# Optimization experiments

Measured on AMD Instinct MI355X. Metric: run time of the kernel, lower is better.

Reference implementation:

```python
import jax, jax.numpy as jnp
import numpy as np

N = 50000
D = 128           # feature_dim
H = 8             # num_heads
DH = D // H       # head_dim = 16
K = 32            # k_neighbors
FFN = int(D * 1.5)  # 192
TAU_NEG = 0.6
BETA = 1.5
LN_EPS = 1e-5


def layer_norm(x, g, b):
    mu = jnp.mean(x, axis=-1, keepdims=True)
    var = jnp.mean((x - mu) ** 2, axis=-1, keepdims=True)
    return (x - mu) * jax.lax.rsqrt(var + LN_EPS) * g + b


def setup_inputs() -> dict:
    key = jax.random.key(0)
    ks = jax.random.split(key, 12)
    s = 1.0 / np.sqrt(D)
    inp = {
        "features": jax.random.normal(ks[0], (N, D), dtype=jnp.float32),
        "knn_indices": jax.random.randint(ks[1], (N, K), 0, N, dtype=jnp.int64 if jax.config.jax_enable_x64 else jnp.int32),
        "spatial_distances": jax.random.uniform(ks[2], (N, K), dtype=jnp.float32) * 8.0,
        "Wq": jax.random.normal(ks[3], (D, D), dtype=jnp.float32) * s,
        "Wk": jax.random.normal(ks[4], (D, D), dtype=jnp.float32) * s,
        "Wv": jax.random.normal(ks[5], (D, D), dtype=jnp.float32) * s,
        "Wo": jax.random.normal(ks[6], (D, D), dtype=jnp.float32) * s,
        "bo": jnp.zeros((D,), dtype=jnp.float32),
        "ln1_g": jnp.ones((D,), dtype=jnp.float32),
        "ln1_b": jnp.zeros((D,), dtype=jnp.float32),
        "W1": jax.random.normal(ks[7], (D, FFN), dtype=jnp.float32) * s,
        "b1": jnp.zeros((FFN,), dtype=jnp.float32),
        "W2": jax.random.normal(ks[8], (FFN, D), dtype=jnp.float32) * (1.0 / np.sqrt(FFN)),
        "b2": jnp.zeros((D,), dtype=jnp.float32),
        "ln2_g": jnp.ones((D,), dtype=jnp.float32),
        "ln2_b": jnp.zeros((D,), dtype=jnp.float32),
    }
    return inp


def reference(features, knn_indices, spatial_distances, Wq, Wk, Wv, Wo, bo,
              ln1_g, ln1_b, W1, b1, W2, b2, ln2_g, ln2_b):
    n = features.shape[0]
    Q = (features @ Wq).reshape(n, H, DH)           # (N,H,dh)
    Kp = (features @ Wk).reshape(n, H, DH)
    Vp = (features @ Wv).reshape(n, H, DH)

    K_local = Kp[knn_indices]                        # (N,K,H,dh) irregular gather
    V_local = Vp[knn_indices]                        # (N,K,H,dh)

    raw_scores = jnp.einsum("nhd,nkhd->nhk", Q, K_local) / np.sqrt(DH)  # (N,H,K)

    # per-head spatial decay: 1 / 2^(h+1)
    head_scalings = (0.5 ** jnp.arange(1, H + 1, dtype=features.dtype))  # (H,)
    scaled_dist = spatial_distances[:, None, :] * head_scalings[None, :, None]  # (N,H,K)

    attn_pos = jax.nn.softmax(raw_scores - scaled_dist, axis=-1)
    attn_neg = jax.nn.softmax((-raw_scores - scaled_dist) / TAU_NEG, axis=-1)
    attn = attn_pos - BETA * attn_neg                # (N,H,K); dropout is identity in eval

    attended = jnp.einsum("nhk,nkhd->nhd", attn, V_local).reshape(n, D)

    x = attended @ Wo + bo + features
    x = layer_norm(x, ln1_g, ln1_b)

    h = jax.nn.gelu(x @ W1 + b1, approximate=False)
    ffn_out = h @ W2 + b2
    out = layer_norm(ffn_out + x, ln2_g, ln2_b)
    return out
```

## Files before the change

### kernel.cpp

```cpp
#include <hip/hip_runtime.h>
#include <hip/hip_fp16.h>
#include <cmath>

typedef __attribute__((ext_vector_type(8))) _Float16 f16x8;
typedef __attribute__((ext_vector_type(4))) float f32x4;

__device__ __forceinline__ unsigned int pkh(float a, float b) {
    __half2 h = __floats2half2_rn(a, b);
    return *(unsigned int*)&h;
}
__device__ __forceinline__ float gelu_exact(float v) {
    return 0.5f * v * (1.0f + erff(v * 0.70710678118654752440f));
}
__device__ __forceinline__ __half2 shfl8h(__half2 x, int m) {
    int xi = *(int*)&x;
    int yi = __shfl_xor(xi, m, 8);
    return *(__half2*)&yi;
}

__global__ __launch_bounds__(256, 1) void k_prep(
    const float* __restrict__ Wq, const float* __restrict__ Wk, const float* __restrict__ Wv,
    const float* __restrict__ Wo, const float* __restrict__ W1, const float* __restrict__ W2,
    unsigned short* __restrict__ wsz)
{
    int f = blockIdx.x * 256 + threadIdx.x;
    const float* W; unsigned short* dst; int M, KS, fl;
    if (f < 2048)       { W = Wq; dst = wsz;         M = 128; KS = 4; fl = f; }
    else if (f < 4096)  { W = Wk; dst = wsz + 16384; M = 128; KS = 4; fl = f - 2048; }
    else if (f < 6144)  { W = Wv; dst = wsz + 32768; M = 128; KS = 4; fl = f - 4096; }
    else if (f < 8192)  { W = Wo; dst = wsz + 49152; M = 128; KS = 4; fl = f - 6144; }
    else if (f < 11264) { W = W1; dst = wsz + 65536; M = 192; KS = 4; fl = f - 8192; }
    else if (f < 14336) { W = W2; dst = wsz + 90112; M = 128; KS = 6; fl = f - 11264; }
    else return;
    const int l  = fl & 63;
    const int ks = (fl >> 6) % KS;
    const int ct = (fl >> 6) / KS;
    const int k0 = ks * 32 + (l >> 4) * 8;
    const int col = ct * 16 + (l & 15);
    unsigned short tmp[8];
    #pragma unroll
    for (int j = 0; j < 8; ++j) {
        __half hh = __float2half(W[(size_t)(k0 + j) * M + col]);
        tmp[j] = *(unsigned short*)&hh;
    }
    ((uint4*)dst)[fl] = *(uint4*)tmp;
}

__global__ __launch_bounds__(256, 4) void k_qkv(
    const float* __restrict__ feat, const unsigned short* __restrict__ wsz,
    unsigned short* __restrict__ Qb, unsigned short* __restrict__ Kb,
    unsigned short* __restrict__ Vb, int n)
{
    const int w = threadIdx.x >> 6, lane = threadIdx.x & 63;
    const int lrow = lane & 15, kgrp = lane >> 4;
    const int node = blockIdx.x * 64 + w * 16 + lrow;
    const bool valid = node < n;

    f16x8 bfr[4];
    #pragma unroll
    for (int ks = 0; ks < 4; ++ks) {
        float4 lo = make_float4(0.f, 0.f, 0.f, 0.f), hi = lo;
        if (valid) {
            const float* p = feat + (size_t)node * 128 + ks * 32 + kgrp * 8;
            lo = *(const float4*)p;
            hi = *(const float4*)(p + 4);
        }
        f16x8 b;
        b[0] = (_Float16)lo.x; b[1] = (_Float16)lo.y; b[2] = (_Float16)lo.z; b[3] = (_Float16)lo.w;
        b[4] = (_Float16)hi.x; b[5] = (_Float16)hi.y; b[6] = (_Float16)hi.z; b[7] = (_Float16)hi.w;
        bfr[ks] = b;
    }

    for (int mat = 0; mat < 3; ++mat) {
        const unsigned short* wb = wsz + mat * 16384;
        f32x4 acc[8];
        #pragma unroll
        for (int ct = 0; ct < 8; ++ct) acc[ct] = (f32x4){0.f, 0.f, 0.f, 0.f};
        #pragma unroll
        for (int ct = 0; ct < 8; ++ct)
            #pragma unroll
            for (int ks = 0; ks < 4; ++ks) {
                f16x8 afr = *(const f16x8*)(wb + ((size_t)(ct * 4 + ks) * 64 + lane) * 8);
                acc[ct] = __builtin_amdgcn_mfma_f32_16x16x32_f16(afr, bfr[ks], acc[ct], 0, 0, 0);
            }
        unsigned short* O = (mat == 0) ? Qb : (mat == 1 ? Kb : Vb);
        if (valid) {
            #pragma unroll
            for (int ct = 0; ct < 8; ++ct) {
                int col = ct * 16 + kgrp * 4;
                *((uint2*)(O + (size_t)node * 128 + col)) =
                    make_uint2(pkh(acc[ct][0], acc[ct][1]), pkh(acc[ct][2], acc[ct][3]));
            }
        }
    }
}

__global__ __launch_bounds__(256, 4) void k_attn(
    const unsigned short* __restrict__ Qb, const unsigned short* __restrict__ Kb,
    const unsigned short* __restrict__ Vb,
    const int* __restrict__ knn, const float* __restrict__ dist,
    unsigned short* __restrict__ attb, int n)
{
    const int lane = threadIdx.x & 63;
    const int node = blockIdx.x * 4 + (threadIdx.x >> 6);
    if (node >= n) return;
    const int h = lane >> 3, r = lane & 7;
    const float hs = exp2f(-(float)(h + 1));

    int idx[4]; float sd[4];
    #pragma unroll
    for (int jj = 0; jj < 4; ++jj) {
        int j = r + jj * 8;
        idx[jj] = knn[(size_t)node * 32 + j];
        sd[jj]  = dist[(size_t)node * 32 + j] * hs;
    }

    const unsigned short* qp = Qb + (size_t)node * 128 + h * 16;
    __half2 q2[8];
    *((uint4*)&q2[0]) = *(const uint4*)qp;
    *((uint4*)&q2[4]) = *(const uint4*)(qp + 8);

    uint4 k0[4], k1[4], v0[4], v1[4];
    #pragma unroll
    for (int jj = 0; jj < 4; ++jj) {
        const unsigned short* kp = Kb + (size_t)idx[jj] * 128 + h * 16;
        k0[jj] = *(const uint4*)kp;
        k1[jj] = *(const uint4*)(kp + 8);
    }
    #pragma unroll
    for (int jj = 0; jj < 4; ++jj) {
        const unsigned short* vp = Vb + (size_t)idx[jj] * 128 + h * 16;
        v0[jj] = *(const uint4*)vp;
        v1[jj] = *(const uint4*)(vp + 8);
    }

    float ap[4], an[4];
    #pragma unroll
    for (int jj = 0; jj < 4; ++jj) {
        const __half2* ka = (const __half2*)&k0[jj];
        const __half2* kb = (const __half2*)&k1[jj];
        __half2 s0 = __hmul2(q2[0], ka[0]);
        s0 = __hfma2(q2[1], ka[1], s0);
        s0 = __hfma2(q2[2], ka[2], s0);
        s0 = __hfma2(q2[3], ka[3], s0);
        __half2 s1 = __hmul2(q2[4], kb[0]);
        s1 = __hfma2(q2[5], kb[1], s1);
        s1 = __hfma2(q2[6], kb[2], s1);
        s1 = __hfma2(q2[7], kb[3], s1);
        float s = __low2float(s0) + __high2float(s0) + __low2float(s1) + __high2float(s1);
        float raw = s * 0.25f;
        ap[jj] = raw - sd[jj];
        an[jj] = (-raw - sd[jj]) * (1.0f / 0.6f);
    }

    float mp = fmaxf(fmaxf(ap[0], ap[1]), fmaxf(ap[2], ap[3]));
    float mn = fmaxf(fmaxf(an[0], an[1]), fmaxf(an[2], an[3]));
    #pragma unroll
    for (int msk = 1; msk < 8; msk <<= 1) {
        mp = fmaxf(mp, __shfl_xor(mp, msk, 8));
        mn = fmaxf(mn, __shfl_xor(mn, msk, 8));
    }
    float ep[4], en[4], sp = 0.f, sn = 0.f;
    #pragma unroll
    for (int jj = 0; jj < 4; ++jj) {
        ep[jj] = expf(ap[jj] - mp); sp += ep[jj];
        en[jj] = expf(an[jj] - mn); sn += en[jj];
    }
    #pragma unroll
    for (int msk = 1; msk < 8; msk <<= 1) {
        sp += __shfl_xor(sp, msk, 8);
        sn += __shfl_xor(sn, msk, 8);
    }
    const float isp = 1.0f / sp;
    const float isn = 1.5f / sn;

    __half2 acc2[8];
    #pragma unroll
    for (int i = 0; i < 8; ++i) acc2[i] = __float2half2_rn(0.f);
    #pragma unroll
    for (int jj = 0; jj < 4; ++jj) {
        float wgt = ep[jj] * isp - en[jj] * isn;
        __half2 w2 = __float2half2_rn(wgt);
        const __half2* va = (const __half2*)&v0[jj];
        const __half2* vb = (const __half2*)&v1[jj];
        acc2[0] = __hfma2(w2, va[0], acc2[0]);
        acc2[1] = __hfma2(w2, va[1], acc2[1]);
        acc2[2] = __hfma2(w2, va[2], acc2[2]);
        acc2[3] = __hfma2(w2, va[3], acc2[3]);
        acc2[4] = __hfma2(w2, vb[0], acc2[4]);
        acc2[5] = __hfma2(w2, vb[1], acc2[5]);
        acc2[6] = __hfma2(w2, vb[2], acc2[6]);
        acc2[7] = __hfma2(w2, vb[3], acc2[7]);
    }
    #pragma unroll
    for (int i = 0; i < 8; ++i) {
        acc2[i] = __hadd2(acc2[i], shfl8h(acc2[i], 1));
        acc2[i] = __hadd2(acc2[i], shfl8h(acc2[i], 2));
        acc2[i] = __hadd2(acc2[i], shfl8h(acc2[i], 4));
    }
    if (r == 0) {
        unsigned short* op = attb + (size_t)node * 128 + h * 16;
        *((uint4*)op)       = *(uint4*)&acc2[0];
        *((uint4*)(op + 8)) = *(uint4*)&acc2[4];
    }
}

__global__ __launch_bounds__(512, 1) void k_tail1(
    const unsigned short* __restrict__ attb, const float* __restrict__ feat,
    const unsigned short* __restrict__ wsz,
    const float* __restrict__ bo, const float* __restrict__ g1, const float* __restrict__ b1ln,
    unsigned short* __restrict__ Xb, int n)
{
    __shared__ __align__(16) unsigned short wo_s[16384];
    const int tid = threadIdx.x;
    for (int i = tid; i < 2048; i += 512)
        ((uint4*)wo_s)[i] = ((const uint4*)(wsz + 49152))[i];

    const int w = tid >> 6, lane = tid & 63;
    const int lrow = lane & 15, kgrp = lane >> 4;
    const int node = blockIdx.x * 128 + w * 16 + lrow;
    const bool valid = node < n;

    f16x8 bfr[4];
    #pragma unroll
    for (int ks = 0; ks < 4; ++ks) {
        uint4 u = make_uint4(0u, 0u, 0u, 0u);
        if (valid) u = *(const uint4*)(attb + (size_t)node * 128 + ks * 32 + kgrp * 8);
        bfr[ks] = *(f16x8*)&u;
    }
    __syncthreads();

    f32x4 X[8];
    #pragma unroll
    for (int ct = 0; ct < 8; ++ct) {
        X[ct] = (f32x4){0.f, 0.f, 0.f, 0.f};
        #pragma unroll
        for (int ks = 0; ks < 4; ++ks) {
            f16x8 afr = *(const f16x8*)&wo_s[((ct * 4 + ks) * 64 + lane) * 8];
            X[ct] = __builtin_amdgcn_mfma_f32_16x16x32_f16(afr, bfr[ks], X[ct], 0, 0, 0);
        }
    }
    #pragma unroll
    for (int ct = 0; ct < 8; ++ct) {
        int col = ct * 16 + kgrp * 4;
        float4 bv = *((const float4*)(bo + col));
        float4 fr = make_float4(0.f, 0.f, 0.f, 0.f);
        if (valid) fr = *((const float4*)(feat + (size_t)node * 128 + col));
        X[ct][0] += bv.x + fr.x; X[ct][1] += bv.y + fr.y;
        X[ct][2] += bv.z + fr.z; X[ct][3] += bv.w + fr.w;
    }
    float s = 0.f;
    #pragma unroll
    for (int ct = 0; ct < 8; ++ct) s += X[ct][0] + X[ct][1] + X[ct][2] + X[ct][3];
    s += __shfl_xor(s, 16); s += __shfl_xor(s, 32);
    const float mu = s * (1.0f / 128.0f);
    float s2 = 0.f;
    #pragma unroll
    for (int ct = 0; ct < 8; ++ct)
        #pragma unroll
        for (int rr = 0; rr < 4; ++rr) { float d = X[ct][rr] - mu; s2 = fmaf(d, d, s2); }
    s2 += __shfl_xor(s2, 16); s2 += __shfl_xor(s2, 32);
    const float rs = rsqrtf(s2 * (1.0f / 128.0f) + 1e-5f);
    if (valid) {
        #pragma unroll
        for (int ct = 0; ct < 8; ++ct) {
            int col = ct * 16 + kgrp * 4;
            float4 gg = *((const float4*)(g1 + col));
            float4 bb = *((const float4*)(b1ln + col));
            float x0 = (X[ct][0] - mu) * rs * gg.x + bb.x;
            float x1 = (X[ct][1] - mu) * rs * gg.y + bb.y;
            float x2 = (X[ct][2] - mu) * rs * gg.z + bb.z;
            float x3 = (X[ct][3] - mu) * rs * gg.w + bb.w;
            *((uint2*)(Xb + (size_t)node * 128 + col)) = make_uint2(pkh(x0, x1), pkh(x2, x3));
        }
    }
}

__global__ __launch_bounds__(512, 1) void k_ffn1(
    const unsigned short* __restrict__ Xb, const unsigned short* __restrict__ wsz,
    const float* __restrict__ b1f, unsigned short* __restrict__ Hb, int n)
{
    __shared__ __align__(16) unsigned short w1_s[24576];
    const int tid = threadIdx.x;
    for (int i = tid; i < 3072; i += 512)
        ((uint4*)w1_s)[i] = ((const uint4*)(wsz + 65536))[i];

    const int w = tid >> 6, lane = tid & 63;
    const int lrow = lane & 15, kgrp = lane >> 4;
    const int node = blockIdx.x * 128 + w * 16 + lrow;
    const bool valid = node < n;

    f16x8 bfr[4];
    #pragma unroll
    for (int ks = 0; ks < 4; ++ks) {
        uint4 u = make_uint4(0u, 0u, 0u, 0u);
        if (valid) u = *(const uint4*)(Xb + (size_t)node * 128 + ks * 32 + kgrp * 8);
        bfr[ks] = *(f16x8*)&u;
    }
    __syncthreads();

    f32x4 acc[12];
    #pragma unroll
    for (int ct = 0; ct < 12; ++ct) {
        acc[ct] = (f32x4){0.f, 0.f, 0.f, 0.f};
        #pragma unroll
        for (int ks = 0; ks < 4; ++ks) {
            f16x8 afr = *(const f16x8*)&w1_s[((ct * 4 + ks) * 64 + lane) * 8];
            acc[ct] = __builtin_amdgcn_mfma_f32_16x16x32_f16(afr, bfr[ks], acc[ct], 0, 0, 0);
        }
    }
    if (valid) {
        #pragma unroll
        for (int ct = 0; ct < 12; ++ct) {
            int col = ct * 16 + kgrp * 4;
            float4 bv = *((const float4*)(b1f + col));
            float h0 = gelu_exact(acc[ct][0] + bv.x);
            float h1 = gelu_exact(acc[ct][1] + bv.y);
            float h2 = gelu_exact(acc[ct][2] + bv.z);
            float h3 = gelu_exact(acc[ct][3] + bv.w);
            *((uint2*)(Hb + (size_t)node * 192 + col)) = make_uint2(pkh(h0, h1), pkh(h2, h3));
        }
    }
}

__global__ __launch_bounds__(512, 1) void k_ffn2(
    const unsigned short* __restrict__ Hb, const unsigned short* __restrict__ Xb,
    const unsigned short* __restrict__ wsz, const float* __restrict__ b2f,
    const float* __restrict__ g2, const float* __restrict__ b2ln,
    float* __restrict__ out, int n)
{
    __shared__ __align__(16) unsigned short w2_s[24576];
    const int tid = threadIdx.x;
    for (int i = tid; i < 3072; i += 512)
        ((uint4*)w2_s)[i] = ((const uint4*)(wsz + 90112))[i];

    const int w = tid >> 6, lane = tid & 63;
    const int lrow = lane & 15, kgrp = lane >> 4;
    const int node = blockIdx.x * 128 + w * 16 + lrow;
    const bool valid = node < n;

    f16x8 bfr[6];
    #pragma unroll
    for (int ks = 0; ks < 6; ++ks) {
        uint4 u = make_uint4(0u, 0u, 0u, 0u);
        if (valid) u = *(const uint4*)(Hb + (size_t)node * 192 + ks * 32 + kgrp * 8);
        bfr[ks] = *(f16x8*)&u;
    }
    __syncthreads();

    f32x4 Y[8];
    #pragma unroll
    for (int ct = 0; ct < 8; ++ct) {
        Y[ct] = (f32x4){0.f, 0.f, 0.f, 0.f};
        #pragma unroll
        for (int ks = 0; ks < 6; ++ks) {
            f16x8 afr = *(const f16x8*)&w2_s[((ct * 6 + ks) * 64 + lane) * 8];
            Y[ct] = __builtin_amdgcn_mfma_f32_16x16x32_f16(afr, bfr[ks], Y[ct], 0, 0, 0);
        }
    }
    #pragma unroll
    for (int ct = 0; ct < 8; ++ct) {
        int col = ct * 16 + kgrp * 4;
        float4 bv = *((const float4*)(b2f + col));
        uint2 xr = make_uint2(0u, 0u);
        if (valid) xr = *((const uint2*)(Xb + (size_t)node * 128 + col));
        __half2 x01 = *(__half2*)&xr.x, x23 = *(__half2*)&xr.y;
        Y[ct][0] += bv.x + __low2float(x01);
        Y[ct][1] += bv.y + __high2float(x01);
        Y[ct][2] += bv.z + __low2float(x23);
        Y[ct][3] += bv.w + __high2float(x23);
    }
    float s = 0.f;
    #pragma unroll
    for (int ct = 0; ct < 8; ++ct) s += Y[ct][0] + Y[ct][1] + Y[ct][2] + Y[ct][3];
    s += __shfl_xor(s, 16); s += __shfl_xor(s, 32);
    const float mu = s * (1.0f / 128.0f);
    float s2 = 0.f;
    #pragma unroll
    for (int ct = 0; ct < 8; ++ct)
        #pragma unroll
        for (int rr = 0; rr < 4; ++rr) { float d = Y[ct][rr] - mu; s2 = fmaf(d, d, s2); }
    s2 += __shfl_xor(s2, 16); s2 += __shfl_xor(s2, 32);
    const float rs = rsqrtf(s2 * (1.0f / 128.0f) + 1e-5f);
    if (valid) {
        #pragma unroll
        for (int ct = 0; ct < 8; ++ct) {
            int col = ct * 16 + kgrp * 4;
            float4 gg = *((const float4*)(g2 + col));
            float4 bb = *((const float4*)(b2ln + col));
            float4 o;
            o.x = (Y[ct][0] - mu) * rs * gg.x + bb.x;
            o.y = (Y[ct][1] - mu) * rs * gg.y + bb.y;
            o.z = (Y[ct][2] - mu) * rs * gg.z + bb.z;
            o.w = (Y[ct][3] - mu) * rs * gg.w + bb.w;
            *((float4*)(out + (size_t)node * 128 + col)) = o;
        }
    }
}

extern "C" void kernel_launch(void* const* d_in, const int* in_sizes, int n_in,
                              void* d_out, int out_size, void* d_ws, size_t ws_size,
                              hipStream_t stream)
{
    const float* feat = (const float*)d_in[0];
    const int*   knn  = (const int*)d_in[1];
    const float* dist = (const float*)d_in[2];
    const float* Wq   = (const float*)d_in[3];
    const float* Wk   = (const float*)d_in[4];
    const float* Wv   = (const float*)d_in[5];
    const float* Wo   = (const float*)d_in[6];
    const float* bo   = (const float*)d_in[7];
    const float* g1   = (const float*)d_in[8];
    const float* b1ln = (const float*)d_in[9];
    const float* W1   = (const float*)d_in[10];
    const float* b1f  = (const float*)d_in[11];
    const float* W2   = (const float*)d_in[12];
    const float* b2f  = (const float*)d_in[13];
    const float* g2   = (const float*)d_in[14];
    const float* b2ln = (const float*)d_in[15];
    float* out = (float*)d_out;

    const int n = in_sizes[0] / 128;
    const size_t ND = (size_t)n * 128;
    if (ws_size < 8 * ND + 262144) return;

    unsigned short* Qb   = (unsigned short*)d_ws;
    unsigned short* Kb   = Qb + ND;
    unsigned short* Vb   = Kb + ND;
    unsigned short* attb = Vb + ND;
    unsigned short* Wsz  = attb + ND;
    unsigned short* Xb   = Vb;
    unsigned short* Hb   = Qb;

    k_prep <<<56, 256, 0, stream>>>(Wq, Wk, Wv, Wo, W1, W2, Wsz);
    k_qkv  <<<(n + 63) / 64,   256, 0, stream>>>(feat, Wsz, Qb, Kb, Vb, n);
    k_attn <<<(n + 3) / 4,     256, 0, stream>>>(Qb, Kb, Vb, knn, dist, attb, n);
    k_tail1<<<(n + 127) / 128, 512, 0, stream>>>(attb, feat, Wsz, bo, g1, b1ln, Xb, n);
    k_ffn1 <<<(n + 127) / 128, 512, 0, stream>>>(Xb, Wsz, b1f, Hb, n);
    k_ffn2 <<<(n + 127) / 128, 512, 0, stream>>>(Hb, Xb, Wsz, b2f, g2, b2ln, out, n);
}
```

Before: 191.0 us.

## Fuse tail kernels, interleave K/V rows, and emit MFMA-ready attention layout

Merges the output projection + LN1, FFN1 + GELU, and FFN2 + LN2 kernels into one kernel. Intermediates now pass through LDS instead of global fp16 buffers, and weights are read straight from global/L2 rather than staged in LDS. K and V are interleaved per node, so each gathered neighbour fetches a single 512-byte contiguous span. The attention output is written in a fragment-swizzled layout that the tail kernel loads directly as MFMA B operands. This cuts launches and global round trips for X and H. The cost is repeated weight reads per wave from cache and different occupancy from 256-thread blocks.

```diff
diff --git a/kernel.cpp b/kernel.cpp
--- a/kernel.cpp
+++ b/kernel.cpp
@@ -48,8 +48,7 @@
 
 __global__ __launch_bounds__(256, 4) void k_qkv(
     const float* __restrict__ feat, const unsigned short* __restrict__ wsz,
-    unsigned short* __restrict__ Qb, unsigned short* __restrict__ Kb,
-    unsigned short* __restrict__ Vb, int n)
+    unsigned short* __restrict__ Qb, unsigned short* __restrict__ KVb, int n)
 {
     const int w = threadIdx.x >> 6, lane = threadIdx.x & 63;
     const int lrow = lane & 15, kgrp = lane >> 4;
@@ -83,12 +82,13 @@
                 f16x8 afr = *(const f16x8*)(wb + ((size_t)(ct * 4 + ks) * 64 + lane) * 8);
                 acc[ct] = __builtin_amdgcn_mfma_f32_16x16x32_f16(afr, bfr[ks], acc[ct], 0, 0, 0);
             }
-        unsigned short* O = (mat == 0) ? Qb : (mat == 1 ? Kb : Vb);
         if (valid) {
+            unsigned short* O = (mat == 0) ? (Qb + (size_t)node * 128)
+                              : (KVb + (size_t)node * 256 + (mat == 2 ? 128 : 0));
             #pragma unroll
             for (int ct = 0; ct < 8; ++ct) {
                 int col = ct * 16 + kgrp * 4;
-                *((uint2*)(O + (size_t)node * 128 + col)) =
+                *((uint2*)(O + col)) =
                     make_uint2(pkh(acc[ct][0], acc[ct][1]), pkh(acc[ct][2], acc[ct][3]));
             }
         }
@@ -96,10 +96,9 @@
 }
 
 __global__ __launch_bounds__(256, 4) void k_attn(
-    const unsigned short* __restrict__ Qb, const unsigned short* __restrict__ Kb,
-    const unsigned short* __restrict__ Vb,
+    const unsigned short* __restrict__ Qb, const unsigned short* __restrict__ KVb,
     const int* __restrict__ knn, const float* __restrict__ dist,
-    unsigned short* __restrict__ attb, int n)
+    unsigned short* __restrict__ attf, int n)
 {
     const int lane = threadIdx.x & 63;
     const int node = blockIdx.x * 4 + (threadIdx.x >> 6);
@@ -123,15 +122,11 @@
     uint4 k0[4], k1[4], v0[4], v1[4];
     #pragma unroll
     for (int jj = 0; jj < 4; ++jj) {
-        const unsigned short* kp = Kb + (size_t)idx[jj] * 128 + h * 16;
-        k0[jj] = *(const uint4*)kp;
-        k1[jj] = *(const uint4*)(kp + 8);
-    }
-    #pragma unroll
-    for (int jj = 0; jj < 4; ++jj) {
-        const unsigned short* vp = Vb + (size_t)idx[jj] * 128 + h * 16;
-        v0[jj] = *(const uint4*)vp;
-        v1[jj] = *(const uint4*)(vp + 8);
+        const unsigned short* kvp = KVb + (size_t)idx[jj] * 256 + h * 16;
+        k0[jj] = *(const uint4*)kvp;
+        k1[jj] = *(const uint4*)(kvp + 8);
+        v0[jj] = *(const uint4*)(kvp + 128);
+        v1[jj] = *(const uint4*)(kvp + 136);
     }
 
     float ap[4], an[4];
@@ -199,44 +194,44 @@
         acc2[i] = __hadd2(acc2[i], shfl8h(acc2[i], 4));
     }
     if (r == 0) {
-        unsigned short* op = attb + (size_t)node * 128 + h * 16;
-        *((uint4*)op)       = *(uint4*)&acc2[0];
-        *((uint4*)(op + 8)) = *(uint4*)&acc2[4];
-    }
-}
-
-__global__ __launch_bounds__(512, 1) void k_tail1(
-    const unsigned short* __restrict__ attb, const float* __restrict__ feat,
+        const int g = node >> 4, lrow = node & 15;
+        unsigned short* op = attf + (size_t)g * 2048 + (h >> 1) * 512 + (h & 1) * 256 + lrow * 8;
+        *((uint4*)op)         = *(uint4*)&acc2[0];
+        *((uint4*)(op + 128)) = *(uint4*)&acc2[4];
+    }
+}
+
+__global__ __launch_bounds__(256, 4) void k_tail(
+    const unsigned short* __restrict__ attf, const float* __restrict__ feat,
     const unsigned short* __restrict__ wsz,
     const float* __restrict__ bo, const float* __restrict__ g1, const float* __restrict__ b1ln,
-    unsigned short* __restrict__ Xb, int n)
-{
-    __shared__ __align__(16) unsigned short wo_s[16384];
+    const float* __restrict__ b1f, const float* __restrict__ b2f,
+    const float* __restrict__ g2, const float* __restrict__ b2ln,
+    float* __restrict__ out, int n)
+{
+    __shared__ __align__(16) unsigned short hls[12288];
     const int tid = threadIdx.x;
-    for (int i = tid; i < 2048; i += 512)
-        ((uint4*)wo_s)[i] = ((const uint4*)(wsz + 49152))[i];
-
     const int w = tid >> 6, lane = tid & 63;
     const int lrow = lane & 15, kgrp = lane >> 4;
-    const int node = blockIdx.x * 128 + w * 16 + lrow;
+    const int node = blockIdx.x * 64 + w * 16 + lrow;
     const bool valid = node < n;
-
-    f16x8 bfr[4];
+    const int g = blockIdx.x * 4 + w;
+
+    f16x8 bfr[6];
     #pragma unroll
     for (int ks = 0; ks < 4; ++ks) {
         uint4 u = make_uint4(0u, 0u, 0u, 0u);
-        if (valid) u = *(const uint4*)(attb + (size_t)node * 128 + ks * 32 + kgrp * 8);
+        if (valid) u = *(const uint4*)(attf + (size_t)g * 2048 + ks * 512 + kgrp * 128 + lrow * 8);
         bfr[ks] = *(f16x8*)&u;
     }
-    __syncthreads();
-
+    const unsigned short* wo = wsz + 49152;
     f32x4 X[8];
     #pragma unroll
     for (int ct = 0; ct < 8; ++ct) {
         X[ct] = (f32x4){0.f, 0.f, 0.f, 0.f};
         #pragma unroll
         for (int ks = 0; ks < 4; ++ks) {
-            f16x8 afr = *(const f16x8*)&wo_s[((ct * 4 + ks) * 64 + lane) * 8];
+            f16x8 afr = *(const f16x8*)(wo + ((size_t)(ct * 4 + ks) * 64 + lane) * 8);
             X[ct] = __builtin_amdgcn_mfma_f32_16x16x32_f16(afr, bfr[ks], X[ct], 0, 0, 0);
         }
     }
@@ -253,108 +248,67 @@
     #pragma unroll
     for (int ct = 0; ct < 8; ++ct) s += X[ct][0] + X[ct][1] + X[ct][2] + X[ct][3];
     s += __shfl_xor(s, 16); s += __shfl_xor(s, 32);
-    const float mu = s * (1.0f / 128.0f);
+    const float mu1 = s * (1.0f / 128.0f);
     float s2 = 0.f;
     #pragma unroll
     for (int ct = 0; ct < 8; ++ct)
         #pragma unroll
-        for (int rr = 0; rr < 4; ++rr) { float d = X[ct][rr] - mu; s2 = fmaf(d, d, s2); }
+        for (int rr = 0; rr < 4; ++rr) { float d = X[ct][rr] - mu1; s2 = fmaf(d, d, s2); }
     s2 += __shfl_xor(s2, 16); s2 += __shfl_xor(s2, 32);
-    const float rs = rsqrtf(s2 * (1.0f / 128.0f) + 1e-5f);
-    if (valid) {
-        #pragma unroll
-        for (int ct = 0; ct < 8; ++ct) {
-            int col = ct * 16 + kgrp * 4;
-            float4 gg = *((const float4*)(g1 + col));
-            float4 bb = *((const float4*)(b1ln + col));
-            float x0 = (X[ct][0] - mu) * rs * gg.x + bb.x;
-            float x1 = (X[ct][1] - mu) * rs * gg.y + bb.y;
-            float x2 = (X[ct][2] - mu) * rs * gg.z + bb.z;
-            float x3 = (X[ct][3] - mu) * rs * gg.w + bb.w;
-            *((uint2*)(Xb + (size_t)node * 128 + col)) = make_uint2(pkh(x0, x1), pkh(x2, x3));
-        }
-    }
-}
-
-__global__ __launch_bounds__(512, 1) void k_ffn1(
-    const unsigned short* __restrict__ Xb, const unsigned short* __restrict__ wsz,
-    const float* __restrict__ b1f, unsigned short* __restrict__ Hb, int n)
-{
-    __shared__ __align__(16) unsigned short w1_s[24576];
-    const int tid = threadIdx.x;
-    for (int i = tid; i < 3072; i += 512)
-        ((uint4*)w1_s)[i] = ((const uint4*)(wsz + 65536))[i];
-
-    const int w = tid >> 6, lane = tid & 63;
-    const int lrow = lane & 15, kgrp = lane >> 4;
-    const int node = blockIdx.x * 128 + w * 16 + lrow;
-    const bool valid = node < n;
-
-    f16x8 bfr[4];
-    #pragma unroll
-    for (int ks = 0; ks < 4; ++ks) {
-        uint4 u = make_uint4(0u, 0u, 0u, 0u);
-        if (valid) u = *(const uint4*)(Xb + (size_t)node * 128 + ks * 32 + kgrp * 8);
-        bfr[ks] = *(f16x8*)&u;
+    const float rs1 = rsqrtf(s2 * (1.0f / 128.0f) + 1e-5f);
+
+    uint2 xnh[8];
+    #pragma unroll
+    for (int ct = 0; ct < 8; ++ct) {
+        int col = ct * 16 + kgrp * 4;
+        float4 gg = *((const float4*)(g1 + col));
+        float4 bb = *((const float4*)(b1ln + col));
+        float x0 = (X[ct][0] - mu1) * rs1 * gg.x + bb.x;
+        float x1 = (X[ct][1] - mu1) * rs1 * gg.y + bb.y;
+        float x2 = (X[ct][2] - mu1) * rs1 * gg.z + bb.z;
+        float x3 = (X[ct][3] - mu1) * rs1 * gg.w + bb.w;
+        xnh[ct] = make_uint2(pkh(x0, x1), pkh(x2, x3));
+        int ks = col >> 5, kg = (col & 31) >> 3, jb = col & 7;
+        *((uint2*)&hls[((w * 4 + ks) * 4 + kg) * 128 + lrow * 8 + jb]) = xnh[ct];
     }
     __syncthreads();
-
-    f32x4 acc[12];
+    #pragma unroll
+    for (int ks = 0; ks < 4; ++ks)
+        bfr[ks] = *(const f16x8*)&hls[((w * 4 + ks) * 4 + kgrp) * 128 + lrow * 8];
+    __syncthreads();
+
+    const unsigned short* w1 = wsz + 65536;
     #pragma unroll
     for (int ct = 0; ct < 12; ++ct) {
-        acc[ct] = (f32x4){0.f, 0.f, 0.f, 0.f};
+        f32x4 acc = (f32x4){0.f, 0.f, 0.f, 0.f};
         #pragma unroll
         for (int ks = 0; ks < 4; ++ks) {
-            f16x8 afr = *(const f16x8*)&w1_s[((ct * 4 + ks) * 64 + lane) * 8];
-            acc[ct] = __builtin_amdgcn_mfma_f32_16x16x32_f16(afr, bfr[ks], acc[ct], 0, 0, 0);
-        }
-    }
-    if (valid) {
-        #pragma unroll
-        for (int ct = 0; ct < 12; ++ct) {
-            int col = ct * 16 + kgrp * 4;
-            float4 bv = *((const float4*)(b1f + col));
-            float h0 = gelu_exact(acc[ct][0] + bv.x);
-            float h1 = gelu_exact(acc[ct][1] + bv.y);
-            float h2 = gelu_exact(acc[ct][2] + bv.z);
-            float h3 = gelu_exact(acc[ct][3] + bv.w);
-            *((uint2*)(Hb + (size_t)node * 192 + col)) = make_uint2(pkh(h0, h1), pkh(h2, h3));
-        }
-    }
-}
-
-__global__ __launch_bounds__(512, 1) void k_ffn2(
-    const unsigned short* __restrict__ Hb, const unsigned short* __restrict__ Xb,
-    const unsigned short* __restrict__ wsz, const float* __restrict__ b2f,
-    const float* __restrict__ g2, const float* __restrict__ b2ln,
-    float* __restrict__ out, int n)
-{
-    __shared__ __align__(16) unsigned short w2_s[24576];
-    const int tid = threadIdx.x;
-    for (int i = tid; i < 3072; i += 512)
-        ((uint4*)w2_s)[i] = ((const uint4*)(wsz + 90112))[i];
-
-    const int w = tid >> 6, lane = tid & 63;
-    const int lrow = lane & 15, kgrp = lane >> 4;
-    const int node = blockIdx.x * 128 + w * 16 + lrow;
-    const bool valid = node < n;
-
-    f16x8 bfr[6];
-    #pragma unroll
-    for (int ks = 0; ks < 6; ++ks) {
-        uint4 u = make_uint4(0u, 0u, 0u, 0u);
-        if (valid) u = *(const uint4*)(Hb + (size_t)node * 192 + ks * 32 + kgrp * 8);
-        bfr[ks] = *(f16x8*)&u;
+            f16x8 afr = *(const f16x8*)(w1 + ((size_t)(ct * 4 + ks) * 64 + lane) * 8);
+            acc = __builtin_amdgcn_mfma_f32_16x16x32_f16(afr, bfr[ks], acc, 0, 0, 0);
+        }
+        int col = ct * 16 + kgrp * 4;
+        float4 bv = *((const float4*)(b1f + col));
+        float h0 = gelu_exact(acc[0] + bv.x);
+        float h1 = gelu_exact(acc[1] + bv.y);
+        float h2 = gelu_exact(acc[2] + bv.z);
+        float h3 = gelu_exact(acc[3] + bv.w);
+        int ks = col >> 5, kg = (col & 31) >> 3, jb = col & 7;
+        *((uint2*)&hls[((w * 6 + ks) * 4 + kg) * 128 + lrow * 8 + jb]) =
+            make_uint2(pkh(h0, h1), pkh(h2, h3));
     }
     __syncthreads();
-
+    #pragma unroll
+    for (int ks = 0; ks < 6; ++ks)
+        bfr[ks] = *(const f16x8*)&hls[((w * 6 + ks) * 4 + kgrp) * 128 + lrow * 8];
+
+    const unsigned short* w2 = wsz + 90112;
     f32x4 Y[8];
     #pragma unroll
     for (int ct = 0; ct < 8; ++ct) {
         Y[ct] = (f32x4){0.f, 0.f, 0.f, 0.f};
         #pragma unroll
         for (int ks = 0; ks < 6; ++ks) {
-            f16x8 afr = *(const f16x8*)&w2_s[((ct * 6 + ks) * 64 + lane) * 8];
+            f16x8 afr = *(const f16x8*)(w2 + ((size_t)(ct * 6 + ks) * 64 + lane) * 8);
             Y[ct] = __builtin_amdgcn_mfma_f32_16x16x32_f16(afr, bfr[ks], Y[ct], 0, 0, 0);
         }
     }
@@ -362,26 +316,24 @@
     for (int ct = 0; ct < 8; ++ct) {
         int col = ct * 16 + kgrp * 4;
         float4 bv = *((const float4*)(b2f + col));
-        uint2 xr = make_uint2(0u, 0u);
-        if (valid) xr = *((const uint2*)(Xb + (size_t)node * 128 + col));
-        __half2 x01 = *(__half2*)&xr.x, x23 = *(__half2*)&xr.y;
+        __half2 x01 = *(__half2*)&xnh[ct].x, x23 = *(__half2*)&xnh[ct].y;
         Y[ct][0] += bv.x + __low2float(x01);
         Y[ct][1] += bv.y + __high2float(x01);
         Y[ct][2] += bv.z + __low2float(x23);
         Y[ct][3] += bv.w + __high2float(x23);
     }
-    float s = 0.f;
-    #pragma unroll
-    for (int ct = 0; ct < 8; ++ct) s += Y[ct][0] + Y[ct][1] + Y[ct][2] + Y[ct][3];
-    s += __shfl_xor(s, 16); s += __shfl_xor(s, 32);
-    const float mu = s * (1.0f / 128.0f);
-    float s2 = 0.f;
+    float t1 = 0.f;
+    #pragma unroll
+    for (int ct = 0; ct < 8; ++ct) t1 += Y[ct][0] + Y[ct][1] + Y[ct][2] + Y[ct][3];
+    t1 += __shfl_xor(t1, 16); t1 += __shfl_xor(t1, 32);
+    const float mu2 = t1 * (1.0f / 128.0f);
+    float t2 = 0.f;
     #pragma unroll
     for (int ct = 0; ct < 8; ++ct)
         #pragma unroll
-        for (int rr = 0; rr < 4; ++rr) { float d = Y[ct][rr] - mu; s2 = fmaf(d, d, s2); }
-    s2 += __shfl_xor(s2, 16); s2 += __shfl_xor(s2, 32);
-    const float rs = rsqrtf(s2 * (1.0f / 128.0f) + 1e-5f);
+        for (int rr = 0; rr < 4; ++rr) { float d = Y[ct][rr] - mu2; t2 = fmaf(d, d, t2); }
+    t2 += __shfl_xor(t2, 16); t2 += __shfl_xor(t2, 32);
+    const float rs2 = rsqrtf(t2 * (1.0f / 128.0f) + 1e-5f);
     if (valid) {
         #pragma unroll
         for (int ct = 0; ct < 8; ++ct) {
@@ -389,10 +341,10 @@
             float4 gg = *((const float4*)(g2 + col));
             float4 bb = *((const float4*)(b2ln + col));
             float4 o;
-            o.x = (Y[ct][0] - mu) * rs * gg.x + bb.x;
-            o.y = (Y[ct][1] - mu) * rs * gg.y + bb.y;
-            o.z = (Y[ct][2] - mu) * rs * gg.z + bb.z;
-            o.w = (Y[ct][3] - mu) * rs * gg.w + bb.w;
+            o.x = (Y[ct][0] - mu2) * rs2 * gg.x + bb.x;
+            o.y = (Y[ct][1] - mu2) * rs2 * gg.y + bb.y;
+            o.z = (Y[ct][2] - mu2) * rs2 * gg.z + bb.z;
+            o.w = (Y[ct][3] - mu2) * rs2 * gg.w + bb.w;
             *((float4*)(out + (size_t)node * 128 + col)) = o;
         }
     }
@@ -425,17 +377,13 @@
     if (ws_size < 8 * ND + 262144) return;
 
     unsigned short* Qb   = (unsigned short*)d_ws;
-    unsigned short* Kb   = Qb + ND;
-    unsigned short* Vb   = Kb + ND;
-    unsigned short* attb = Vb + ND;
-    unsigned short* Wsz  = attb + ND;
-    unsigned short* Xb   = Vb;
-    unsigned short* Hb   = Qb;
-
-    k_prep <<<56, 256, 0, stream>>>(Wq, Wk, Wv, Wo, W1, W2, Wsz);
-    k_qkv  <<<(n + 63) / 64,   256, 0, stream>>>(feat, Wsz, Qb, Kb, Vb, n);
-    k_attn <<<(n + 3) / 4,     256, 0, stream>>>(Qb, Kb, Vb, knn, dist, attb, n);
-    k_tail1<<<(n + 127) / 128, 512, 0, stream>>>(attb, feat, Wsz, bo, g1, b1ln, Xb, n);
-    k_ffn1 <<<(n + 127) / 128, 512, 0, stream>>>(Xb, Wsz, b1f, Hb, n);
-    k_ffn2 <<<(n + 127) / 128, 512, 0, stream>>>(Hb, Xb, Wsz, b2f, g2, b2ln, out, n);
-}
+    unsigned short* KVb  = Qb + ND;
+    unsigned short* attf = KVb + 2 * ND;
+    unsigned short* Wsz  = attf + ND;
+
+    k_prep<<<56, 256, 0, stream>>>(Wq, Wk, Wv, Wo, W1, W2, Wsz);
+    k_qkv <<<(n + 63) / 64, 256, 0, stream>>>(feat, Wsz, Qb, KVb, n);
+    k_attn<<<(n + 3) / 4,   256, 0, stream>>>(Qb, KVb, knn, dist, attf, n);
+    k_tail<<<(n + 63) / 64, 256, 0, stream>>>(attf, feat, Wsz, bo, g1, b1ln, b1f, b2f,
+                                              g2, b2ln, out, n);
+}
```

New measurement: 179.8 us. -5.8%, faster.
